# Performance work log

Measured on AMD Instinct MI355X. Metric: run time of the kernel, lower is better.

Reference implementation:

```python
import jax, jax.numpy as jnp
import numpy as np

B, N, C = 16, 8192, 384   # batch, points, feature dim
G, M = 512, 32            # num_group (FPS centers), group_size (KNN k)


def setup_inputs() -> dict:
    key = jax.random.key(0)
    k1, k2 = jax.random.split(key)
    xyz = jax.random.normal(k1, (B, N, 3), dtype=jnp.float32)
    features = jax.random.normal(k2, (B, N, C), dtype=jnp.float32)
    return {"xyz": xyz, "features": features}


def _fps(xyz, n_samples):
    """Farthest point sampling, deterministic start at index 0 (matches CUDA op).
    xyz: [B, N, 3] -> idx: [B, n_samples] int32."""
    b, n, _ = xyz.shape
    big = jnp.asarray(1e10, xyz.dtype)

    def step(carry, _):
        min_dist, farthest = carry
        centroid = jnp.take_along_axis(xyz, farthest[:, None, None], axis=1)  # [B,1,3]
        d = jnp.sum((xyz - centroid) ** 2, axis=-1)                            # [B,N]
        min_dist = jnp.minimum(min_dist, d)
        nxt = jnp.argmax(min_dist, axis=-1).astype(jnp.int32)
        return (min_dist, nxt), farthest

    init = (jnp.full((b, n), big, xyz.dtype), jnp.zeros((b,), jnp.int32))
    _, idxs = jax.lax.scan(step, init, None, length=n_samples)  # [G, B]
    return jnp.transpose(idxs)  # [B, G]


def _knn_idx(ref, query, k):
    """Indices of k nearest ref points for each query. ref [B,N,3], query [B,G,3] -> [B,G,k]."""
    d = (jnp.sum(query ** 2, -1)[..., None]
         + jnp.sum(ref ** 2, -1)[:, None, :]
         - 2.0 * jnp.einsum('bgd,bnd->bgn', query, ref))  # [B,G,N]
    _, idx = jax.lax.top_k(-d, k)
    return idx


def reference(xyz, features):
    fps_idx = _fps(xyz, G)                                        # [B,G]
    center = jnp.take_along_axis(xyz, fps_idx[..., None], axis=1)  # [B,G,3]
    idx = _knn_idx(xyz, center, M)                                 # [B,G,M]

    gather = jax.vmap(lambda pts, i: pts[i])                       # per-batch fancy gather
    flat_idx = idx.reshape(B, G * M)
    neighborhood = gather(xyz, flat_idx).reshape(B, G, M, 3)
    feature_group = gather(features, flat_idx).reshape(B, G, M, C)
    neighborhood = neighborhood - center[:, :, None, :]
    return neighborhood, center, feature_group
```

## Files before the change

### kernel.cpp

```cpp
#include <hip/hip_runtime.h>
#include <math.h>

#define BATCH 16
#define NPTS  8192
#define FEATC 384
#define NG    512
#define KM    32

#define OUT0_OFF 0
#define OUT1_OFF (BATCH * NG * KM * 3)
#define OUT2_OFF (OUT1_OFF + BATCH * NG * 3)

#pragma clang fp contract(off)

typedef float f32x2 __attribute__((ext_vector_type(2)));
typedef float f32x4 __attribute__((ext_vector_type(4)));

template <int CTRL>
__device__ __forceinline__ int dpp1(int x) {
    return __builtin_amdgcn_update_dpp(x, x, CTRL, 0xF, 0xF, false);
}

__device__ __forceinline__ unsigned long long wave_max_u64(unsigned long long k) {
    unsigned long long o;
#define STEP(C)                                                                \
    {                                                                          \
        unsigned lo = (unsigned)dpp1<C>((int)(unsigned)k);                     \
        unsigned hi = (unsigned)dpp1<C>((int)(unsigned)(k >> 32));             \
        o = ((unsigned long long)hi << 32) | lo;                               \
        if (o > k) k = o;                                                      \
    }
    STEP(0x111) STEP(0x112) STEP(0x114) STEP(0x118) STEP(0x142) STEP(0x143)
#undef STEP
    return k;
}

__device__ __forceinline__ unsigned long long wave_min_u64(unsigned long long k) {
    unsigned long long o;
#define STEP(C)                                                                \
    {                                                                          \
        unsigned lo = (unsigned)dpp1<C>((int)(unsigned)k);                     \
        unsigned hi = (unsigned)dpp1<C>((int)(unsigned)(k >> 32));             \
        o = ((unsigned long long)hi << 32) | lo;                               \
        if (o < k) k = o;                                                      \
    }
    STEP(0x111) STEP(0x112) STEP(0x114) STEP(0x118) STEP(0x142) STEP(0x143)
#undef STEP
    return k;
}

__device__ __forceinline__ unsigned long long min16_u64(const unsigned long long* k) {
    unsigned long long t8[8];
#pragma unroll
    for (int i = 0; i < 8; ++i) t8[i] = k[i] < k[i + 8] ? k[i] : k[i + 8];
    unsigned long long t4[4];
#pragma unroll
    for (int i = 0; i < 4; ++i) t4[i] = t8[i] < t8[i + 4] ? t8[i] : t8[i + 4];
    unsigned long long a = t4[0] < t4[2] ? t4[0] : t4[2];
    unsigned long long b = t4[1] < t4[3] ? t4[1] : t4[3];
    return a < b ? a : b;
}

__global__ void init_progress(int* progress) {
    if (threadIdx.x < BATCH)
        __hip_atomic_store(&progress[threadIdx.x], 0,
                           __ATOMIC_RELAXED, __HIP_MEMORY_SCOPE_AGENT);
}

__global__ __launch_bounds__(512) void group_kernel(const float* __restrict__ xyz,
                                                    const float* __restrict__ features,
                                                    float* __restrict__ out0,
                                                    float* __restrict__ out1,
                                                    float* __restrict__ out2,
                                                    int* __restrict__ progress) {
#pragma clang fp contract(off)
    __shared__ unsigned long long sk[2][8];
    __shared__ int   sidx[KM];
    __shared__ float scst[24];

    const int tid  = threadIdx.x;
    const int lane = tid & 63;
    const int wid  = tid >> 6;

    if (blockIdx.x < BATCH) {
        __builtin_amdgcn_s_setprio(3);
        const int b = blockIdx.x;
        const float* xb = xyz + (size_t)b * NPTS * 3;
        float* co = out1 + (size_t)b * NG * 3;

        f32x2 X[8], Y[8], Z[8], MD[8];
#pragma unroll
        for (int j = 0; j < 8; ++j) {
            int p0 = tid + 1024 * j;
            int p1 = p0 + 512;
            X[j]  = (f32x2){xb[p0 * 3 + 0], xb[p1 * 3 + 0]};
            Y[j]  = (f32x2){xb[p0 * 3 + 1], xb[p1 * 3 + 1]};
            Z[j]  = (f32x2){xb[p0 * 3 + 2], xb[p1 * 3 + 2]};
            MD[j] = (f32x2){1e10f, 1e10f};
        }

        int far = 0;
        for (int g = 0; g < NG; ++g) {
            const float cx = xb[far * 3 + 0];
            const float cy = xb[far * 3 + 1];
            const float cz = xb[far * 3 + 2];
            if (tid == 0) {
                scst[(g & 7) * 3 + 0] = cx;
                scst[(g & 7) * 3 + 1] = cy;
                scst[(g & 7) * 3 + 2] = cz;
            }
            const f32x2 cx2 = (f32x2){cx, cx};
            const f32x2 cy2 = (f32x2){cy, cy};
            const f32x2 cz2 = (f32x2){cz, cz};

#pragma unroll
            for (int j = 0; j < 8; ++j) {
                f32x2 dx = X[j] - cx2;
                f32x2 dy = Y[j] - cy2;
                f32x2 dz = Z[j] - cz2;
                f32x2 d  = (dx * dx + dy * dy) + dz * dz;
                MD[j] = __builtin_elementwise_min(MD[j], d);
            }
            f32x2 a0 = __builtin_elementwise_max(MD[0], MD[1]);
            f32x2 a1 = __builtin_elementwise_max(MD[2], MD[3]);
            f32x2 a2 = __builtin_elementwise_max(MD[4], MD[5]);
            f32x2 a3 = __builtin_elementwise_max(MD[6], MD[7]);
            f32x2 b0 = __builtin_elementwise_max(a0, a1);
            f32x2 b1 = __builtin_elementwise_max(a2, a3);
            f32x2 c0 = __builtin_elementwise_max(b0, b1);
            float lmax = fmaxf(c0.x, c0.y);

            unsigned candX = 0xFFFFFFFFu, candY = 0xFFFFFFFFu;
#pragma unroll
            for (int j = 7; j >= 0; --j) {
                if (MD[j].y == lmax) candY = (unsigned)(tid + 1024 * j + 512);
                if (MD[j].x == lmax) candX = (unsigned)(tid + 1024 * j);
            }
            unsigned cand = candX < candY ? candX : candY;

            unsigned long long key =
                ((unsigned long long)__float_as_uint(lmax) << 32) | (unsigned)(~cand);
            key = wave_max_u64(key);

            const int par = g & 1;
            if (lane == 63) sk[par][wid] = key;
            __syncthreads();

            unsigned long long m0 = sk[par][0] > sk[par][1] ? sk[par][0] : sk[par][1];
            unsigned long long m1 = sk[par][2] > sk[par][3] ? sk[par][2] : sk[par][3];
            unsigned long long m2 = sk[par][4] > sk[par][5] ? sk[par][4] : sk[par][5];
            unsigned long long m3 = sk[par][6] > sk[par][7] ? sk[par][6] : sk[par][7];
            unsigned long long ma = m0 > m1 ? m0 : m1;
            unsigned long long mb = m2 > m3 ? m2 : m3;
            unsigned long long gk = ma > mb ? ma : mb;
            far = (int)(~(unsigned)gk);

            if ((g & 7) == 7) {
                if (tid < 24) co[(g - 7) * 3 + tid] = scst[tid];
                if (tid == 0)
                    __hip_atomic_store(&progress[b], g + 1,
                                       __ATOMIC_RELEASE, __HIP_MEMORY_SCOPE_AGENT);
            }
        }
        return;
    }

    const int i = blockIdx.x - BATCH;
    const int b = i & 15;
    const int g = i >> 4;
    const int bgrow = b * NG + g;

    if (tid == 0) {
        while ((int)__hip_atomic_load(&progress[b], __ATOMIC_ACQUIRE,
                                      __HIP_MEMORY_SCOPE_AGENT) < g + 1)
            __builtin_amdgcn_s_sleep(127);
        unsigned* co = (unsigned*)out1 + (size_t)bgrow * 3;
        scst[0] = __uint_as_float(__hip_atomic_load(co + 0, __ATOMIC_RELAXED,
                                                    __HIP_MEMORY_SCOPE_AGENT));
        scst[1] = __uint_as_float(__hip_atomic_load(co + 1, __ATOMIC_RELAXED,
                                                    __HIP_MEMORY_SCOPE_AGENT));
        scst[2] = __uint_as_float(__hip_atomic_load(co + 2, __ATOMIC_RELAXED,
                                                    __HIP_MEMORY_SCOPE_AGENT));
    }
    __syncthreads();

    const float cx = scst[0], cy = scst[1], cz = scst[2];
    const float q2 = (cx * cx + cy * cy) + cz * cz;

    const float* xb = xyz + (size_t)b * NPTS * 3;

    unsigned long long k[16];
#pragma unroll
    for (int j = 0; j < 16; ++j) {
        int p = tid + (j << 9);
        float rx = xb[p * 3 + 0];
        float ry = xb[p * 3 + 1];
        float rz = xb[p * 3 + 2];
        float r2 = (rx * rx + ry * ry) + rz * rz;
        float dot = fmaf(cz, rz, fmaf(cy, ry, cx * rx));
        float d = (q2 + r2) - 2.0f * dot;
        unsigned u = __float_as_uint(d);
        u ^= ((unsigned)((int)u >> 31)) | 0x80000000u;
        k[j] = ((unsigned long long)u << 32) | (unsigned)p;
    }

    unsigned long long lv = min16_u64(k);
    unsigned long long wkey = wave_min_u64(lv);
    if (lane == 63) sk[0][wid] = wkey;
    __syncthreads();

    for (int kk = 0; kk < KM; ++kk) {
        const int par = kk & 1;
        const int nxt = par ^ 1;
        unsigned long long m0 = sk[par][0] < sk[par][1] ? sk[par][0] : sk[par][1];
        unsigned long long m1 = sk[par][2] < sk[par][3] ? sk[par][2] : sk[par][3];
        unsigned long long m2 = sk[par][4] < sk[par][5] ? sk[par][4] : sk[par][5];
        unsigned long long m3 = sk[par][6] < sk[par][7] ? sk[par][6] : sk[par][7];
        unsigned long long ma = m0 < m1 ? m0 : m1;
        unsigned long long mb = m2 < m3 ? m2 : m3;
        unsigned long long gk = ma < mb ? ma : mb;
        const unsigned pt = (unsigned)gk;
        const int wwave = (int)((pt & 511u) >> 6);

        if (wid == wwave) {
            if ((pt & 511u) == (unsigned)tid) {
                sidx[kk] = (int)pt;
                const unsigned jw = pt >> 9;
#pragma unroll
                for (int j = 0; j < 16; ++j) {
                    if ((unsigned)j == jw) k[j] = ~0ULL;
                }
                lv = min16_u64(k);
            }
            wkey = wave_min_u64(lv);
            if (lane == 63) sk[nxt][wid] = wkey;
        } else {
            if (lane == 63) sk[nxt][wid] = wkey;
        }
        __syncthreads();
    }

    if (tid < 96) {
        int m = tid / 3;
        int c = tid - 3 * m;
        int p = sidx[m];
        float v = xb[p * 3 + c] - scst[c];
        __builtin_nontemporal_store(v, &out0[((size_t)bgrow * KM + m) * 3 + c]);
    }

    const f32x4* fb = (const f32x4*)(features + (size_t)b * NPTS * FEATC);
    f32x4*       ob = (f32x4*)(out2 + (size_t)bgrow * KM * FEATC);
#pragma unroll
    for (int r = 0; r < 6; ++r) {
        int flat = tid + (r << 9);
        int m  = flat / 96;
        int c4 = flat - 96 * m;
        f32x4 v = __builtin_nontemporal_load(&fb[(size_t)sidx[m] * 96 + c4]);
        __builtin_nontemporal_store(v, &ob[(size_t)m * 96 + c4]);
    }
}

extern "C" void kernel_launch(void* const* d_in, const int* in_sizes, int n_in,
                              void* d_out, int out_size, void* d_ws, size_t ws_size,
                              hipStream_t stream) {
    const float* xyz      = (const float*)d_in[0];
    const float* features = (const float*)d_in[1];
    float* out  = (float*)d_out;
    float* out0 = out + OUT0_OFF;
    float* out1 = out + OUT1_OFF;
    float* out2 = out + OUT2_OFF;

    int* progress = (int*)d_ws;

    init_progress<<<1, 64, 0, stream>>>(progress);
    group_kernel<<<BATCH + BATCH * NG, 512, 0, stream>>>(xyz, features,
                                                         out0, out1, out2,
                                                         progress);
}
```

Measured before the change: 626.8 us.

## Reload contiguous xyz chunks per FPS iteration instead of holding coordinates in registers

The FPS block now gives each thread 16 contiguous points, read as 12 float4 loads, and reloads them from global/L1 on every iteration instead of keeping X/Y/Z in registers for all 512 steps. This frees registers and uses wide vector loads, at the cost of repeated memory traffic inside the serial FPS loop. The candidate index calculation changes to match the new contiguous point mapping, and the s_setprio raise for the FPS blocks is removed.

```diff
diff --git a/kernel.cpp b/kernel.cpp
--- a/kernel.cpp
+++ b/kernel.cpp
@@ -83,24 +83,20 @@
     const int wid  = tid >> 6;
 
     if (blockIdx.x < BATCH) {
-        __builtin_amdgcn_s_setprio(3);
         const int b = blockIdx.x;
         const float* xb = xyz + (size_t)b * NPTS * 3;
         float* co = out1 + (size_t)b * NG * 3;
-
-        f32x2 X[8], Y[8], Z[8], MD[8];
-#pragma unroll
-        for (int j = 0; j < 8; ++j) {
-            int p0 = tid + 1024 * j;
-            int p1 = p0 + 512;
-            X[j]  = (f32x2){xb[p0 * 3 + 0], xb[p1 * 3 + 0]};
-            Y[j]  = (f32x2){xb[p0 * 3 + 1], xb[p1 * 3 + 1]};
-            Z[j]  = (f32x2){xb[p0 * 3 + 2], xb[p1 * 3 + 2]};
-            MD[j] = (f32x2){1e10f, 1e10f};
-        }
+        const f32x4* cb = (const f32x4*)(xb + 48 * tid);
+
+        f32x2 MD[8];
+#pragma unroll
+        for (int u = 0; u < 8; ++u) MD[u] = (f32x2){1e10f, 1e10f};
 
         int far = 0;
         for (int g = 0; g < NG; ++g) {
+            f32x4 A0 = cb[0], A1 = cb[1], A2 = cb[2];
+            f32x4 B0 = cb[3], B1 = cb[4], B2 = cb[5];
+
             const float cx = xb[far * 3 + 0];
             const float cy = xb[far * 3 + 1];
             const float cz = xb[far * 3 + 2];
@@ -114,13 +110,27 @@
             const f32x2 cz2 = (f32x2){cz, cz};
 
 #pragma unroll
-            for (int j = 0; j < 8; ++j) {
-                f32x2 dx = X[j] - cx2;
-                f32x2 dy = Y[j] - cy2;
-                f32x2 dz = Z[j] - cz2;
-                f32x2 d  = (dx * dx + dy * dy) + dz * dz;
-                MD[j] = __builtin_elementwise_min(MD[j], d);
-            }
+            for (int c = 0; c < 4; ++c) {
+                f32x2 xl = (f32x2){A0.x, A0.w};
+                f32x2 yl = (f32x2){A0.y, A1.x};
+                f32x2 zl = (f32x2){A0.z, A1.y};
+                f32x2 xh = (f32x2){A1.z, A2.y};
+                f32x2 yh = (f32x2){A1.w, A2.z};
+                f32x2 zh = (f32x2){A2.x, A2.w};
+                A0 = B0; A1 = B1; A2 = B2;
+                if (c < 2) {
+                    B0 = cb[3 * c + 6];
+                    B1 = cb[3 * c + 7];
+                    B2 = cb[3 * c + 8];
+                }
+                f32x2 dxl = xl - cx2, dyl = yl - cy2, dzl = zl - cz2;
+                f32x2 dl  = (dxl * dxl + dyl * dyl) + dzl * dzl;
+                MD[2 * c] = __builtin_elementwise_min(MD[2 * c], dl);
+                f32x2 dxh = xh - cx2, dyh = yh - cy2, dzh = zh - cz2;
+                f32x2 dh  = (dxh * dxh + dyh * dyh) + dzh * dzh;
+                MD[2 * c + 1] = __builtin_elementwise_min(MD[2 * c + 1], dh);
+            }
+
             f32x2 a0 = __builtin_elementwise_max(MD[0], MD[1]);
             f32x2 a1 = __builtin_elementwise_max(MD[2], MD[3]);
             f32x2 a2 = __builtin_elementwise_max(MD[4], MD[5]);
@@ -130,13 +140,12 @@
             f32x2 c0 = __builtin_elementwise_max(b0, b1);
             float lmax = fmaxf(c0.x, c0.y);
 
-            unsigned candX = 0xFFFFFFFFu, candY = 0xFFFFFFFFu;
-#pragma unroll
-            for (int j = 7; j >= 0; --j) {
-                if (MD[j].y == lmax) candY = (unsigned)(tid + 1024 * j + 512);
-                if (MD[j].x == lmax) candX = (unsigned)(tid + 1024 * j);
-            }
-            unsigned cand = candX < candY ? candX : candY;
+            unsigned cand = 0xFFFFFFFFu;
+#pragma unroll
+            for (int u = 7; u >= 0; --u) {
+                if (MD[u].y == lmax) cand = (unsigned)(16 * tid + 2 * u + 1);
+                if (MD[u].x == lmax) cand = (unsigned)(16 * tid + 2 * u);
+            }
 
             unsigned long long key =
                 ((unsigned long long)__float_as_uint(lmax) << 32) | (unsigned)(~cand);
```

Result: no change. 620.2 us, median of 2 (-1.0%).
